# Optimization experiments

Hardware: AMD Instinct MI355X
Metric: run time of the kernel (lower is better)

The kernel has to match this reference:

```python
import jax, jax.numpy as jnp
import numpy as np

B, T, E, H = 8, 2048, 512, 16
D = E // H  # 32 embeddings per head
LN_EPS = 1e-3  # keras LayerNormalization default epsilon
DECAY = 1.2


def setup_inputs() -> dict:
    key = jax.random.key(0)
    k0, k1, k2 = jax.random.split(key, 3)
    x = jax.random.normal(k0, (B, T, E), dtype=jnp.float32)
    W = jax.random.normal(k1, (E, E), dtype=jnp.float32) * (1.0 / np.sqrt(E))
    b = jnp.zeros((E,), dtype=jnp.float32)
    concept_map = jax.random.normal(k2, (H, D, D, D), dtype=jnp.float32) * 0.02
    gamma = jnp.ones((E,), dtype=jnp.float32)
    beta = jnp.zeros((E,), dtype=jnp.float32)
    return {"x": x, "W": W, "b": b, "concept_map": concept_map,
            "gamma": gamma, "beta": beta}


def reference(x, W, b, concept_map, gamma, beta):
    Bn, Tn, En = x.shape
    Hn = concept_map.shape[0]
    Dn = En // Hn
    # Dense projection, split into heads: (B,T,H,D)
    h = (jnp.einsum('bte,ef->btf', x, W) + b).reshape(Bn, Tn, Hn, Dn)
    # Decayed cumulative sum of preceding tokens: S_0 = 0, S_t = (S_{t-1} + h_{t-1}) / 1.2
    def step(s, h_t):
        return (s + h_t) / DECAY, s
    _, S = jax.lax.scan(step, jnp.zeros((Bn, Hn, Dn), h.dtype),
                        jnp.swapaxes(h, 0, 1))  # S: (T,B,H,D)
    S = jnp.swapaxes(S, 0, 1)  # (B,T,H,D)
    # Fused bilinear contraction: sum_{i,j} h[...,i] * S[...,j] * C[h,k,i,j]
    # (equivalent to outer-product * concept_map then reduce_sum over last two dims)
    y = jnp.einsum('bthi,bthj,hkij->bthk', h, S, concept_map) + h
    y = y.reshape(Bn, Tn, En)
    # LayerNormalization over last axis (keras default eps=1e-3)
    mu = jnp.mean(y, axis=-1, keepdims=True)
    var = jnp.var(y, axis=-1, keepdims=True)
    y = (y - mu) * jax.lax.rsqrt(var + LN_EPS) * gamma + beta
    # Dropout: identity at inference
    return y
```

## Files before the change

kernel.cpp:

```cpp
#include <hip/hip_runtime.h>
#include <hip/hip_bf16.h>

#define Bn 8
#define Tn 2048
#define En 512
#define Hn 16
#define Dn 32
#define NC 32
#define CL 64
#define NT (Bn*Tn)
#define INV_DECAY (1.0f/1.2f)

typedef __attribute__((ext_vector_type(8))) short  bf16x8;
typedef __attribute__((ext_vector_type(4))) float  f32x4;
typedef __attribute__((ext_vector_type(8))) unsigned short u16x8;

__device__ __forceinline__ unsigned short f2b(float f) {
    __hip_bfloat16 h = __float2bfloat16(f);
    return *reinterpret_cast<unsigned short*>(&h);
}
__device__ __forceinline__ float b2f(unsigned short u) {
    union { unsigned int i; float f; } c; c.i = ((unsigned int)u) << 16; return c.f;
}

__host__ __device__ constexpr float wpow(int e) {
    float r = 1.f;
    for (int i = 0; i < e; i++) r *= (1.0f / 1.2f);
    return r;
}

__device__ __forceinline__ size_t hm(int hd, int tok, int ch) {
    return (size_t)hd * ((size_t)NT * Dn) + (size_t)tok * Dn + ch;
}

__global__ __launch_bounds__(256) void prep_k(const float* __restrict__ C,
                                              unsigned short* __restrict__ Cl,
                                              const float* __restrict__ W,
                                              unsigned short* __restrict__ Wt) {
    __shared__ float tile[32][33];
    if (blockIdx.x < 256) {
        const int g = blockIdx.x * 256 + threadIdx.x;
        const int hd = g >> 12, rem = g & 4095;
        const int i = rem >> 7, half = (rem >> 6) & 1, lane = rem & 63;
        const int tloc = lane & 15, kgrp = lane >> 4;
        const int k = half * 16 + tloc;
        const float* src = C + (size_t)hd * 32768 + (size_t)k * 1024 + i * 32 + kgrp * 8;
        float4 a = reinterpret_cast<const float4*>(src)[0];
        float4 b = reinterpret_cast<const float4*>(src)[1];
        u16x8 st;
        st[0]=f2b(a.x); st[1]=f2b(a.y); st[2]=f2b(a.z); st[3]=f2b(a.w);
        st[4]=f2b(b.x); st[5]=f2b(b.y); st[6]=f2b(b.z); st[7]=f2b(b.w);
        *reinterpret_cast<u16x8*>(Cl + (size_t)g * 8) = st;
    } else {
        const int bid = blockIdx.x - 256;
        const int kb = (bid & 15) * 32, nb = (bid >> 4) * 32;
        const int tx = threadIdx.x & 31, ty = threadIdx.x >> 5;
        #pragma unroll
        for (int j = 0; j < 4; j++)
            tile[ty + 8 * j][tx] = W[(size_t)(kb + ty + 8 * j) * En + nb + tx];
        __syncthreads();
        #pragma unroll
        for (int j = 0; j < 4; j++)
            Wt[(size_t)(nb + ty + 8 * j) * En + kb + tx] = f2b(tile[tx][ty + 8 * j]);
    }
}

__global__ __launch_bounds__(256) void gemm_mfma_k(const float* __restrict__ x,
                                                   const unsigned short* __restrict__ Wt,
                                                   const float* __restrict__ bias,
                                                   unsigned short* __restrict__ h,
                                                   float* __restrict__ locals) {
    __shared__ unsigned short As[128][40];
    __shared__ unsigned short Bs[64][40];
    const int m0 = blockIdx.x * 128, n0 = blockIdx.y * 64;
    const int tid = threadIdx.x;
    const int wid = tid >> 6, lane = tid & 63;
    const int tloc = lane & 15, kgrp = lane >> 4;
    const int wr = wid >> 1, wc = wid & 1;

    const int ar = tid >> 1, ah = (tid & 1) * 16;
    const int brr = tid >> 2, bq = (tid & 3) * 8;

    f32x4 acc[4][2] = {};

    for (int k0 = 0; k0 < En; k0 += 32) {
        const float* xp = &x[(size_t)(m0 + ar) * En + k0 + ah];
        float4 a0 = reinterpret_cast<const float4*>(xp)[0];
        float4 a1 = reinterpret_cast<const float4*>(xp)[1];
        float4 a2 = reinterpret_cast<const float4*>(xp)[2];
        float4 a3 = reinterpret_cast<const float4*>(xp)[3];
        u16x8 bv = *reinterpret_cast<const u16x8*>(&Wt[(size_t)(n0 + brr) * En + k0 + bq]);
        __syncthreads();
        u16x8 w0, w1;
        w0[0]=f2b(a0.x); w0[1]=f2b(a0.y); w0[2]=f2b(a0.z); w0[3]=f2b(a0.w);
        w0[4]=f2b(a1.x); w0[5]=f2b(a1.y); w0[6]=f2b(a1.z); w0[7]=f2b(a1.w);
        w1[0]=f2b(a2.x); w1[1]=f2b(a2.y); w1[2]=f2b(a2.z); w1[3]=f2b(a2.w);
        w1[4]=f2b(a3.x); w1[5]=f2b(a3.y); w1[6]=f2b(a3.z); w1[7]=f2b(a3.w);
        *reinterpret_cast<u16x8*>(&As[ar][ah])     = w0;
        *reinterpret_cast<u16x8*>(&As[ar][ah + 8]) = w1;
        *reinterpret_cast<u16x8*>(&Bs[brr][bq])    = bv;
        __syncthreads();

        bf16x8 afr[4], bfr[2];
        #pragma unroll
        for (int m = 0; m < 4; m++)
            afr[m] = *reinterpret_cast<const bf16x8*>(&As[wr * 64 + m * 16 + tloc][kgrp * 8]);
        #pragma unroll
        for (int n = 0; n < 2; n++)
            bfr[n] = *reinterpret_cast<const bf16x8*>(&Bs[wc * 32 + n * 16 + tloc][kgrp * 8]);
        #pragma unroll
        for (int m = 0; m < 4; m++)
            #pragma unroll
            for (int n = 0; n < 2; n++)
                acc[m][n] = __builtin_amdgcn_mfma_f32_16x16x32_bf16(afr[m], bfr[n], acc[m][n], 0, 0, 0);
    }

    const float kmul = (kgrp & 1 ? 2.0736f : 1.f) * (kgrp & 2 ? 4.29981696f : 1.f);
    const int cg = blockIdx.x * 2 + wr;

    #pragma unroll
    for (int n = 0; n < 2; n++) {
        const int col = n0 + wc * 32 + n * 16 + tloc;
        const float bcol = bias[col];
        const int hd = col >> 5, ch = col & 31;
        float part = 0.f;
        #pragma unroll
        for (int m = 0; m < 4; m++)
            #pragma unroll
            for (int r = 0; r < 4; r++) {
                const int row = m0 + wr * 64 + m * 16 + kgrp * 4 + r;
                const unsigned short hb16 = f2b(acc[m][n][r] + bcol);
                h[hm(hd, row, ch)] = hb16;
                part += b2f(hb16) * (wpow(64 - m * 16 - r) * kmul);
            }
        part += __shfl_xor(part, 16);
        part += __shfl_xor(part, 32);
        if (kgrp == 0) locals[(size_t)cg * En + col] = part;
    }
}

__global__ __launch_bounds__(512) void scan_prefix_k(const float* __restrict__ locals,
                                                     float* __restrict__ Acar) {
    const int b = blockIdx.x;
    const int e = threadIdx.x;
    float invRL = 1.f;
    #pragma unroll
    for (int i = 0; i < CL; i++) invRL *= INV_DECAY;
    float A = 0.f;
    for (int c = 0; c < NC; c++) {
        Acar[(size_t)(b * NC + c) * En + e] = A;
        A = A * invRL + locals[(size_t)(b * NC + c) * En + e];
    }
}

__global__ __launch_bounds__(512) void scan_emit_k(const unsigned short* __restrict__ h,
                                                   const float* __restrict__ Acar,
                                                   unsigned short* __restrict__ Sg) {
    const int c = blockIdx.x, b = blockIdx.y;
    const int e = threadIdx.x;
    const int hd = e >> 5, ch = e & 31;
    float s = Acar[(size_t)(b * NC + c) * En + e];
    const size_t base = hm(hd, b * Tn + c * CL, ch);
    for (int t = 0; t < CL; t++) {
        Sg[base + (size_t)t * Dn] = f2b(s);
        s = (s + b2f(h[base + (size_t)t * Dn])) * INV_DECAY;
    }
}

__global__ __launch_bounds__(256, 4) void bilinear12_k(const unsigned short* __restrict__ hg,
                                                       const unsigned short* __restrict__ Sg,
                                                       unsigned short* __restrict__ yb,
                                                       const unsigned short* __restrict__ Cl) {
    __shared__ float ys[4][64][36];

    const int hd = blockIdx.y;
    const int tid = threadIdx.x;
    const int wid = tid >> 6, lane = tid & 63;
    const int tloc = lane & 15, kgrp = lane >> 4;
    const int j0 = kgrp * 8;
    const int tokens0 = blockIdx.x * 64;

    bf16x8 afr[8][2];
    {
        const unsigned short* cb = Cl + (size_t)hd * 32768;
        #pragma unroll
        for (int s = 0; s < 8; s++) {
            const int i = wid * 8 + s;
            #pragma unroll
            for (int mt = 0; mt < 2; mt++)
                afr[s][mt] = *reinterpret_cast<const bf16x8*>(
                    cb + ((size_t)((i * 2 + mt) * 64 + lane) * 8));
        }
    }

    u16x8 hreg[4];
    float sf[4][8];
    #pragma unroll
    for (int nt = 0; nt < 4; nt++) {
        const int trow = tokens0 + nt * 16 + tloc;
        hreg[nt] = *reinterpret_cast<const u16x8*>(hg + hm(hd, trow, wid * 8));
        u16x8 sv = *reinterpret_cast<const u16x8*>(Sg + hm(hd, trow, j0));
        #pragma unroll
        for (int e = 0; e < 8; e++) sf[nt][e] = b2f(sv[e]);
    }

    f32x4 acc[2][4] = {};
    #pragma unroll
    for (int s = 0; s < 8; s++) {
        #pragma unroll
        for (int nt = 0; nt < 4; nt++) {
            const float hsc = b2f(hreg[nt][s]);
            bf16x8 bfrag;
            #pragma unroll
            for (int e = 0; e < 8; e++) bfrag[e] = (short)f2b(hsc * sf[nt][e]);
            acc[0][nt] = __builtin_amdgcn_mfma_f32_16x16x32_bf16(afr[s][0], bfrag, acc[0][nt], 0, 0, 0);
            acc[1][nt] = __builtin_amdgcn_mfma_f32_16x16x32_bf16(afr[s][1], bfrag, acc[1][nt], 0, 0, 0);
        }
    }

    #pragma unroll
    for (int mt = 0; mt < 2; mt++)
        #pragma unroll
        for (int nt = 0; nt < 4; nt++)
            *reinterpret_cast<f32x4*>(&ys[wid][nt * 16 + tloc][mt * 16 + kgrp * 4]) = acc[mt][nt];
    __syncthreads();

    {
        const int token = tid >> 2, q = tid & 3;
        f32x4 y0 = {0.f,0.f,0.f,0.f}, y1 = {0.f,0.f,0.f,0.f};
        #pragma unroll
        for (int w = 0; w < 4; w++) {
            const f32x4* src = reinterpret_cast<const f32x4*>(&ys[w][token][q * 8]);
            y0 += src[0];
            y1 += src[1];
        }
        u16x8 hres = *reinterpret_cast<const u16x8*>(hg + hm(hd, tokens0 + token, q * 8));
        u16x8 st;
        #pragma unroll
        for (int e = 0; e < 4; e++) {
            st[e]     = f2b(y0[e] + b2f(hres[e]));
            st[4 + e] = f2b(y1[e] + b2f(hres[4 + e]));
        }
        *reinterpret_cast<u16x8*>(yb + hm(hd, tokens0 + token, q * 8)) = st;
    }
}

__global__ __launch_bounds__(256) void ln_k(const unsigned short* __restrict__ y,
                                            const float* __restrict__ gamma,
                                            const float* __restrict__ beta,
                                            float* __restrict__ out) {
    const int row = blockIdx.x * 4 + (threadIdx.x >> 6);
    const int lane = threadIdx.x & 63;
    u16x8 v = *reinterpret_cast<const u16x8*>(y + hm(lane >> 2, row, (lane & 3) * 8));
    float f[8];
    float s = 0.f, s2 = 0.f;
    #pragma unroll
    for (int e = 0; e < 8; e++) {
        f[e] = b2f(v[e]);
        s += f[e]; s2 += f[e] * f[e];
    }
    #pragma unroll
    for (int off = 1; off < 64; off <<= 1) {
        s  += __shfl_xor(s, off);
        s2 += __shfl_xor(s2, off);
    }
    const float mu = s * (1.f / En);
    const float var = s2 * (1.f / En) - mu * mu;
    const float rs = rsqrtf(var + 1e-3f);
    const int cbase = lane * 8;
    float4 g0 = reinterpret_cast<const float4*>(&gamma[cbase])[0];
    float4 g1 = reinterpret_cast<const float4*>(&gamma[cbase])[1];
    float4 b0 = reinterpret_cast<const float4*>(&beta[cbase])[0];
    float4 b1 = reinterpret_cast<const float4*>(&beta[cbase])[1];
    float4 o0, o1;
    o0.x = (f[0] - mu) * rs * g0.x + b0.x; o0.y = (f[1] - mu) * rs * g0.y + b0.y;
    o0.z = (f[2] - mu) * rs * g0.z + b0.z; o0.w = (f[3] - mu) * rs * g0.w + b0.w;
    o1.x = (f[4] - mu) * rs * g1.x + b1.x; o1.y = (f[5] - mu) * rs * g1.y + b1.y;
    o1.z = (f[6] - mu) * rs * g1.z + b1.z; o1.w = (f[7] - mu) * rs * g1.w + b1.w;
    float* op = out + (size_t)row * En;
    reinterpret_cast<float4*>(op)[lane * 2]     = o0;
    reinterpret_cast<float4*>(op)[lane * 2 + 1] = o1;
}

extern "C" void kernel_launch(void* const* d_in, const int* in_sizes, int n_in,
                              void* d_out, int out_size, void* d_ws, size_t ws_size,
                              hipStream_t stream) {
    const float* x     = (const float*)d_in[0];
    const float* W     = (const float*)d_in[1];
    const float* bias  = (const float*)d_in[2];
    const float* C     = (const float*)d_in[3];
    const float* gamma = (const float*)d_in[4];
    const float* beta  = (const float*)d_in[5];
    float* out = (float*)d_out;

    unsigned short* hb  = (unsigned short*)d_ws;
    unsigned short* Sg  = hb + (size_t)Hn * NT * Dn;
    unsigned short* Cl  = Sg + (size_t)Hn * NT * Dn;
    unsigned short* Wt  = Cl + (size_t)Hn * Dn * Dn * Dn;
    float* locals = (float*)(Wt + (size_t)En * En);
    float* Acar   = locals + (size_t)Bn * NC * En;

    prep_k<<<512, 256, 0, stream>>>(C, Cl, W, Wt);
    gemm_mfma_k<<<dim3(NT / 128, En / 64), 256, 0, stream>>>(x, Wt, bias, hb, locals);
    scan_prefix_k<<<Bn, 512, 0, stream>>>(locals, Acar);
    scan_emit_k<<<dim3(NC, Bn), 512, 0, stream>>>(hb, Acar, Sg);
    bilinear12_k<<<dim3(NT / CL, Hn), 256, 0, stream>>>(hb, Sg, Sg , Cl);
    ln_k<<<NT / 4, 256, 0, stream>>>(Sg, gamma, beta, out);
}
```

Measured before the change: 81.91 us.

## Stage GEMM output through LDS for vector stores; merge scan prefix into emit kernel

The GEMM epilogue now writes its bf16 tile into shared memory and then stores it to the head-major h buffer as 16-byte vectors, replacing the scattered 2-byte stores. The separate chunk-prefix scan kernel is removed. Each emit block instead recomputes its carry-in by summing the earlier chunks' locals with decay weights, and the emit scan uses 8-wide vector loads and stores with 64 threads per block. This drops one kernel launch and the Acar round trip. In exchange it adds redundant prefix work that grows with chunk index, extra LDS in the GEMM, and a much smaller emit grid (256 blocks of 64 threads).

```diff
diff --git a/kernel.cpp b/kernel.cpp
--- a/kernel.cpp
+++ b/kernel.cpp
@@ -72,6 +72,7 @@
                                                    float* __restrict__ locals) {
     __shared__ unsigned short As[128][40];
     __shared__ unsigned short Bs[64][40];
+    __shared__ unsigned short Ht[128][72];
     const int m0 = blockIdx.x * 128, n0 = blockIdx.y * 64;
     const int tid = threadIdx.x;
     const int wid = tid >> 6, lane = tid & 63;
@@ -121,49 +122,61 @@
     #pragma unroll
     for (int n = 0; n < 2; n++) {
         const int col = n0 + wc * 32 + n * 16 + tloc;
+        const int lcol = wc * 32 + n * 16 + tloc;
         const float bcol = bias[col];
-        const int hd = col >> 5, ch = col & 31;
         float part = 0.f;
         #pragma unroll
         for (int m = 0; m < 4; m++)
             #pragma unroll
             for (int r = 0; r < 4; r++) {
-                const int row = m0 + wr * 64 + m * 16 + kgrp * 4 + r;
                 const unsigned short hb16 = f2b(acc[m][n][r] + bcol);
-                h[hm(hd, row, ch)] = hb16;
+                Ht[wr * 64 + m * 16 + kgrp * 4 + r][lcol] = hb16;
                 part += b2f(hb16) * (wpow(64 - m * 16 - r) * kmul);
             }
         part += __shfl_xor(part, 16);
         part += __shfl_xor(part, 32);
         if (kgrp == 0) locals[(size_t)cg * En + col] = part;
     }
-}
-
-__global__ __launch_bounds__(512) void scan_prefix_k(const float* __restrict__ locals,
-                                                     float* __restrict__ Acar) {
-    const int b = blockIdx.x;
-    const int e = threadIdx.x;
-    float invRL = 1.f;
-    #pragma unroll
-    for (int i = 0; i < CL; i++) invRL *= INV_DECAY;
-    float A = 0.f;
-    for (int c = 0; c < NC; c++) {
-        Acar[(size_t)(b * NC + c) * En + e] = A;
-        A = A * invRL + locals[(size_t)(b * NC + c) * En + e];
-    }
-}
-
-__global__ __launch_bounds__(512) void scan_emit_k(const unsigned short* __restrict__ h,
-                                                   const float* __restrict__ Acar,
+    __syncthreads();
+
+    {
+        const int row = tid >> 1, half = tid & 1;
+        const int hd = (n0 >> 5) + half;
+        #pragma unroll
+        for (int q = 0; q < 4; q++) {
+            u16x8 v = *reinterpret_cast<const u16x8*>(&Ht[row][half * 32 + q * 8]);
+            *reinterpret_cast<u16x8*>(h + hm(hd, m0 + row, q * 8)) = v;
+        }
+    }
+}
+
+__global__ __launch_bounds__(64) void scan_emit2_k(const unsigned short* __restrict__ h,
+                                                   const float* __restrict__ locals,
                                                    unsigned short* __restrict__ Sg) {
     const int c = blockIdx.x, b = blockIdx.y;
-    const int e = threadIdx.x;
-    const int hd = e >> 5, ch = e & 31;
-    float s = Acar[(size_t)(b * NC + c) * En + e];
+    const int g = threadIdx.x;
+    const int hd = g >> 2, ch = (g & 3) * 8;
+    constexpr float INVRL = wpow(64);
+
+    float A[8] = {0.f, 0.f, 0.f, 0.f, 0.f, 0.f, 0.f, 0.f};
+    float w = 1.f;
+    for (int cp = c - 1; cp >= 0; --cp) {
+        const float* lp = &locals[(size_t)(b * NC + cp) * En + hd * Dn + ch];
+        #pragma unroll
+        for (int e = 0; e < 8; e++) A[e] += w * lp[e];
+        w *= INVRL;
+    }
+
     const size_t base = hm(hd, b * Tn + c * CL, ch);
     for (int t = 0; t < CL; t++) {
-        Sg[base + (size_t)t * Dn] = f2b(s);
-        s = (s + b2f(h[base + (size_t)t * Dn])) * INV_DECAY;
+        u16x8 hv = *reinterpret_cast<const u16x8*>(h + base + (size_t)t * Dn);
+        u16x8 sv;
+        #pragma unroll
+        for (int e = 0; e < 8; e++) {
+            sv[e] = f2b(A[e]);
+            A[e] = (A[e] + b2f(hv[e])) * INV_DECAY;
+        }
+        *reinterpret_cast<u16x8*>(Sg + base + (size_t)t * Dn) = sv;
     }
 }
 
@@ -298,12 +311,10 @@
     unsigned short* Cl  = Sg + (size_t)Hn * NT * Dn;
     unsigned short* Wt  = Cl + (size_t)Hn * Dn * Dn * Dn;
     float* locals = (float*)(Wt + (size_t)En * En);
-    float* Acar   = locals + (size_t)Bn * NC * En;
 
     prep_k<<<512, 256, 0, stream>>>(C, Cl, W, Wt);
     gemm_mfma_k<<<dim3(NT / 128, En / 64), 256, 0, stream>>>(x, Wt, bias, hb, locals);
-    scan_prefix_k<<<Bn, 512, 0, stream>>>(locals, Acar);
-    scan_emit_k<<<dim3(NC, Bn), 512, 0, stream>>>(hb, Acar, Sg);
+    scan_emit2_k<<<dim3(NC, Bn), 64, 0, stream>>>(hb, locals, Sg);
     bilinear12_k<<<dim3(NT / CL, Hn), 256, 0, stream>>>(hb, Sg, Sg , Cl);
     ln_k<<<NT / 4, 256, 0, stream>>>(Sg, gamma, beta, out);
 }
```

After: 92.71 us. +13.2%, slower.
